# Kernel tuning notes

Hardware: AMD Instinct MI355X
Metric: run time of the kernel (lower is better)

Reference implementation:

```python
import jax, jax.numpy as jnp
import numpy as np

N_NODES = 20000
N_EDGES = 100000
MUL = 128          # channels per irrep
R = 8              # radial (edge scalar) features
H = 64             # radial MLP hidden width
SILU_NORM = 1.6790390826      # e3nn normalize2mom constant for SiLU
INV_SQRT3 = 1.0 / np.sqrt(3.0)   # wigner-3j values for l<=1 paths
PW_0E = np.sqrt(0.5)   # e3nn path weight: out dim 1, fan-in 2 paths
PW_1O = np.sqrt(1.5)   # e3nn path weight: out dim 3, fan-in 2 paths


def setup_inputs() -> dict:
    key = jax.random.key(0)
    ks = jax.random.split(key, 12)
    return dict(
        node_feats=jax.random.normal(ks[0], (N_NODES, 4 * MUL), jnp.float32),
        edge_attrs=jax.random.normal(ks[1], (N_EDGES, 4), jnp.float32),   # SH: 1x0e+1x1o
        edge_feats=jax.random.normal(ks[2], (N_EDGES, R), jnp.float32),
        edge_index=jax.random.randint(ks[3], (2, N_EDGES), 0, N_NODES),
        W_up_s=jax.random.normal(ks[4], (MUL, MUL), jnp.float32),
        W_up_v=jax.random.normal(ks[5], (MUL, MUL), jnp.float32),
        mlp_w0=jax.random.normal(ks[6], (R, H), jnp.float32),
        mlp_w1=jax.random.normal(ks[7], (H, H), jnp.float32),
        mlp_w2=jax.random.normal(ks[8], (H, H), jnp.float32),
        mlp_w3=jax.random.normal(ks[9], (H, 4 * MUL), jnp.float32),
        W_out_s=jax.random.normal(ks[10], (2 * MUL, MUL), jnp.float32),
        W_out_v=jax.random.normal(ks[11], (2 * MUL, MUL), jnp.float32),
    )


def reference(node_feats, edge_attrs, edge_feats, edge_index,
              W_up_s, W_up_v, mlp_w0, mlp_w1, mlp_w2, mlp_w3,
              W_out_s, W_out_v):
    sender = edge_index[0]
    # split node feats into irrep blocks: 128x0e then 128x1o (channel-major [u, m])
    s = node_feats[:, :MUL]                       # [N, 128]
    v = node_feats[:, MUL:].reshape(-1, MUL, 3)   # [N, 128, 3]
    # linear_up: per-irrep e3nn Linear, fan_in-normalized
    s = (s @ W_up_s) / np.sqrt(MUL)
    v = jnp.einsum('nui,uw->nwi', v, W_up_v) / np.sqrt(MUL)
    # radial MLP -> per-edge tensor-product weights (e3nn FullyConnectedNet)
    act = lambda x: jax.nn.silu(x) * SILU_NORM
    h = act(edge_feats @ (mlp_w0 / np.sqrt(R)))
    h = act(h @ (mlp_w1 / np.sqrt(H)))
    h = act(h @ (mlp_w2 / np.sqrt(H)))
    tpw = h @ (mlp_w3 / np.sqrt(H))               # [E, 4*128]
    w00, w01, w10, w11 = jnp.split(tpw, 4, axis=1)  # instruction order of weight_numel
    # gather sender node features per edge
    ss = s[sender]                                # [E, 128]
    vs = v[sender]                                # [E, 128, 3]
    sh0 = edge_attrs[:, :1]                       # [E, 1]  scalar SH
    sh1 = edge_attrs[:, 1:]                       # [E, 3]  l=1 SH
    # uvu CG tensor product paths (l<=1 wigner-3j)
    a0 = PW_0E * w00 * ss * sh0                                   # 0e x 0e -> 0e
    a1 = (PW_1O * INV_SQRT3) * (w01 * ss)[:, :, None] * sh1[:, None, :]   # 0e x 1o -> 1o
    b1 = (PW_1O * INV_SQRT3) * (w10 * sh0)[:, :, None] * vs              # 1o x 0e -> 1o
    b0 = (PW_0E * INV_SQRT3) * w11 * jnp.einsum('eui,ei->eu', vs, sh1)   # 1o x 1o -> 0e
    # irreps_mid sorted+simplified: 256x0e + 256x1o
    mid_s = jnp.concatenate([a0, b0], axis=1)     # [E, 256]
    mid_v = jnp.concatenate([a1, b1], axis=1)     # [E, 256, 3]
    # final per-irrep linear to target 128x0e + 128x1o
    out_s = (mid_s @ W_out_s) / np.sqrt(2 * MUL)
    out_v = jnp.einsum('eui,uw->ewi', mid_v, W_out_v) / np.sqrt(2 * MUL)
    return jnp.concatenate([out_s, out_v.reshape(out_v.shape[0], 3 * MUL)], axis=1)
```

## Files before the change

kernel.cpp:

```cpp
#include <hip/hip_runtime.h>
#include <stdint.h>

#define N_NODES 20000
#define N_EDGES 100000

typedef __bf16 bf16;
typedef bf16  bf16x8 __attribute__((ext_vector_type(8)));
typedef float f32x4  __attribute__((ext_vector_type(4)));

__device__ __forceinline__ f32x4 mfma16(bf16x8 a, bf16x8 b, f32x4 c) {
  return __builtin_amdgcn_mfma_f32_16x16x32_bf16(a, b, c, 0, 0, 0);
}

__device__ __forceinline__ float silu_(float y) {
  return y / (1.0f + __expf(-y));
}

#define OFF_W0T   0u
#define OFF_W1T   4096u
#define OFF_W2T   12288u
#define OFF_W3T   20480u
#define OFF_WOS   86016u
#define OFF_WOV   151552u
#define OFF_WST   217088u
#define OFF_WVT   249856u
#define OFF_SUP   282624u
#define OFF_VUP   5402624u

__global__ __launch_bounds__(256) void k0_prep(
    const float* __restrict__ wus, const float* __restrict__ wuv,
    const float* __restrict__ w0,  const float* __restrict__ w1,
    const float* __restrict__ w2,  const float* __restrict__ w3,
    const float* __restrict__ wos_g, const float* __restrict__ wov_g,
    char* __restrict__ ws) {
  const int idx = blockIdx.x * 256 + threadIdx.x;
  bf16* W0T = (bf16*)(ws + OFF_W0T);
  bf16* W1T = (bf16*)(ws + OFF_W1T);
  bf16* W2T = (bf16*)(ws + OFF_W2T);
  bf16* W3T = (bf16*)(ws + OFF_W3T);
  bf16* WOS = (bf16*)(ws + OFF_WOS);
  bf16* WOV = (bf16*)(ws + OFF_WOV);
  bf16* WST = (bf16*)(ws + OFF_WST);
  bf16* WVT = (bf16*)(ws + OFF_WVT);

  const float cS   = 0.08838834764831845f;
  const float c0   = 0.35355339059327373f;
  const float c12  = 1.6790390826f / 8.0f;
  const float cosA = 0.04419417382415922f;
  const float cosB = 0.025515518153991442f;
  const float cov  = 0.04419417382415922f;

  if (idx < 16384) {
    int w = idx >> 7, u = idx & 127;
    WST[idx] = (bf16)(wus[u * 128 + w] * cS);
    WVT[idx] = (bf16)(wuv[u * 128 + w] * cS);
  }
  if (idx < 2048) {
    int h = idx >> 5, r = idx & 31;
    W0T[idx] = (bf16)((r < 8) ? w0[r * 64 + h] * c0 : 0.0f);
  }
  if (idx < 4096) {
    int h = idx >> 6, k = idx & 63;
    W1T[idx] = (bf16)(w1[k * 64 + h] * c12);
    W2T[idx] = (bf16)(w2[k * 64 + h] * c12);
  }
  {
    int j = idx >> 6, k = idx & 63;
    W3T[idx] = (bf16)(w3[k * 512 + j] * c12);
    int w = idx >> 8, u = idx & 255;
    WOS[idx] = (bf16)(wos_g[u * 128 + w] * ((u < 128) ? cosA : cosB));
    WOV[idx] = (bf16)(wov_g[u * 128 + w] * cov);
  }
}

__global__ __launch_bounds__(256, 4) void k1_nodeup(const float* __restrict__ nf,
                                                    char* __restrict__ ws) {
  __shared__ __align__(16) bf16 tiles[4][32 * 136];
  const int n0 = blockIdx.x * 32;
  const int t = threadIdx.x;

  #pragma unroll
  for (int p = 0; p < 16; p++) {
    int idx = p * 256 + t;
    int r = idx >> 7, c4 = idx & 127;
    const float4 f = *(const float4*)&nf[(size_t)(n0 + r) * 512 + c4 * 4];
    float vals[4] = {f.x, f.y, f.z, f.w};
    #pragma unroll
    for (int e2 = 0; e2 < 4; e2++) {
      int g = c4 * 4 + e2;
      if (g < 128) {
        tiles[0][r * 136 + g] = (bf16)vals[e2];
      } else {
        int gg = g - 128;
        int u = gg / 3, i = gg - 3 * u;
        tiles[1 + i][r * 136 + u] = (bf16)vals[e2];
      }
    }
  }
  __syncthreads();

  const int wv = t >> 6, lane = t & 63;
  const int m = lane & 15, q = lane >> 4;
  const bf16* BT = (const bf16*)(ws + ((wv == 0) ? OFF_WST : OFF_WVT));
  const bf16* At = tiles[wv];

  const f32x4 z = {0.f, 0.f, 0.f, 0.f};
  f32x4 acc[2][8] = {{z, z, z, z, z, z, z, z}, {z, z, z, z, z, z, z, z}};
  #pragma unroll
  for (int kk = 0; kk < 128; kk += 32) {
    bf16x8 af0 = *(const bf16x8*)&At[m * 136 + kk + q * 8];
    bf16x8 af1 = *(const bf16x8*)&At[(16 + m) * 136 + kk + q * 8];
    #pragma unroll
    for (int nt = 0; nt < 8; nt++) {
      bf16x8 bfr = *(const bf16x8*)&BT[(nt * 16 + m) * 128 + kk + q * 8];
      acc[0][nt] = mfma16(af0, bfr, acc[0][nt]);
      acc[1][nt] = mfma16(af1, bfr, acc[1][nt]);
    }
  }

  bf16* sup = (bf16*)(ws + OFF_SUP);
  bf16* vup = (bf16*)(ws + OFF_VUP);
  #pragma unroll
  for (int rt = 0; rt < 2; rt++) {
    #pragma unroll
    for (int nt = 0; nt < 8; nt++) {
      int col = nt * 16 + m;
      #pragma unroll
      for (int r = 0; r < 4; r++) {
        int node = n0 + rt * 16 + q * 4 + r;
        if (wv == 0) sup[node * 128 + col] = (bf16)acc[rt][nt][r];
        else         vup[node * 384 + (wv - 1) * 128 + col] = (bf16)acc[rt][nt][r];
      }
    }
  }
}

#define L_TPW   0
#define L_H0    0
#define L_H1    4608
#define L_SUP   16896
#define L_VUP   25088
#define L_TOT   49664
#define TPW_LD  264

#define GLOAD_LDS16(gsrc, ldst) __builtin_amdgcn_global_load_lds( \
    (const __attribute__((address_space(1))) void*)(gsrc),        \
    (__attribute__((address_space(3))) void*)(ldst), 16, 0, 0)

__device__ __forceinline__ bf16x8 ldsw8(const bf16* row, int elem, int sw) {
  int c = elem >> 3;
  int cs = (c & ~7) | ((c ^ sw) & 7);
  return *(const bf16x8*)&row[cs * 8];
}

__device__ __forceinline__ bf16x8 build_frag(
    int wv, int ii, int kc, int off ,
    const bf16* tpr, const bf16* supR, const bf16* vupR, int sw,
    float4 at, float s1i) {
  bf16x8 af;
  if (kc < 2) {
    const int K = kc * 64 + off;
    bf16x8 sv = ldsw8(supR, K, sw);
    if (wv == 0) {
      bf16x8 tv = *(const bf16x8*)&tpr[K];
      #pragma unroll
      for (int j = 0; j < 8; j++)
        af[j] = (bf16)((float)tv[j] * (float)sv[j] * at.x);
    } else {
      bf16x8 tv = *(const bf16x8*)&tpr[128 + K];
      #pragma unroll
      for (int j = 0; j < 8; j++)
        af[j] = (bf16)((float)tv[j] * (float)sv[j] * s1i);
    }
  } else {
    const int Kl = (kc - 2) * 64 + off;
    if (wv == 0) {
      bf16x8 tv = *(const bf16x8*)&tpr[128 + Kl];
      bf16x8 vx = ldsw8(vupR, Kl, sw);
      bf16x8 vy = ldsw8(vupR, 128 + Kl, sw);
      bf16x8 vz = ldsw8(vupR, 256 + Kl, sw);
      #pragma unroll
      for (int j = 0; j < 8; j++) {
        float dv = (float)vx[j] * at.y + (float)vy[j] * at.z + (float)vz[j] * at.w;
        af[j] = (bf16)((float)tv[j] * dv);
      }
    } else {
      bf16x8 tv = *(const bf16x8*)&tpr[Kl];
      bf16x8 vv = ldsw8(vupR, ii * 128 + Kl, sw);
      #pragma unroll
      for (int j = 0; j < 8; j++)
        af[j] = (bf16)((float)tv[j] * at.x * (float)vv[j]);
    }
  }
  return af;
}

__global__ __launch_bounds__(256, 3) void k23_fused(
    const float* __restrict__ efeat, const float* __restrict__ attrs,
    const int* __restrict__ sender, const char* __restrict__ ws,
    float* __restrict__ out) {
  __shared__ __align__(16) char smem[L_TOT];
  bf16* tpwH = (bf16*)(smem + L_TPW);
  bf16* h0   = (bf16*)(smem + L_H0);
  bf16* h1   = (bf16*)(smem + L_H1);
  bf16* supL = (bf16*)(smem + L_SUP);
  bf16* vupL = (bf16*)(smem + L_VUP);

  const int e0 = blockIdx.x * 32;
  const int t = threadIdx.x;
  const int wv = t >> 6, lane = t & 63;
  const int m = lane & 15, q = lane >> 4;
  const f32x4 z = {0.f, 0.f, 0.f, 0.f};

  {
    #pragma unroll
    for (int jj = 0; jj < 2; jj++) {
      int j = wv * 2 + jj;
      int f = j * 64 + lane;
      int e = f >> 4, c = f & 15;
      int se = sender[e0 + e];
      int cs = c ^ (e & 7);
      GLOAD_LDS16(ws + OFF_SUP + (size_t)se * 256 + cs * 16,
                  (char*)supL + j * 1024);
    }
    #pragma unroll
    for (int jj = 0; jj < 6; jj++) {
      int j = wv * 6 + jj;
      int f = j * 64 + lane;
      int e = f / 48, c = f - e * 48;
      int se = sender[e0 + e];
      int cs = (c & ~7) | ((c ^ e) & 7);
      GLOAD_LDS16(ws + OFF_VUP + (size_t)se * 768 + cs * 16,
                  (char*)vupL + j * 1024);
    }
  }

  const bf16* W0T = (const bf16*)(ws + OFF_W0T);
  const bf16* W1T = (const bf16*)(ws + OFF_W1T);
  const bf16* W2T = (const bf16*)(ws + OFF_W2T);
  const bf16* W3T = (const bf16*)(ws + OFF_W3T);

  const int rt = wv & 1, nh = wv >> 1;

  {
    bf16x8 af;
    #pragma unroll
    for (int j = 0; j < 8; j++) af[j] = (bf16)0.0f;
    if (q == 0) {
      const float4* ef4 = (const float4*)efeat;
      float4 u0 = ef4[(size_t)(e0 + rt * 16 + m) * 2 + 0];
      float4 u1 = ef4[(size_t)(e0 + rt * 16 + m) * 2 + 1];
      af[0] = (bf16)u0.x; af[1] = (bf16)u0.y; af[2] = (bf16)u0.z; af[3] = (bf16)u0.w;
      af[4] = (bf16)u1.x; af[5] = (bf16)u1.y; af[6] = (bf16)u1.z; af[7] = (bf16)u1.w;
    }
    f32x4 acc[2] = {z, z};
    #pragma unroll
    for (int ntl = 0; ntl < 2; ntl++) {
      bf16x8 bfr = *(const bf16x8*)&W0T[((nh * 2 + ntl) * 16 + m) * 32 + q * 8];
      acc[ntl] = mfma16(af, bfr, acc[ntl]);
    }
    #pragma unroll
    for (int ntl = 0; ntl < 2; ntl++)
      #pragma unroll
      for (int r = 0; r < 4; r++)
        h0[(rt * 16 + q * 4 + r) * 72 + (nh * 2 + ntl) * 16 + m] = (bf16)silu_(acc[ntl][r]);
  }
  __syncthreads();

  {
    f32x4 acc[2] = {z, z};
    #pragma unroll
    for (int kk = 0; kk < 64; kk += 32) {
      bf16x8 af = *(const bf16x8*)&h0[(rt * 16 + m) * 72 + kk + q * 8];
      #pragma unroll
      for (int ntl = 0; ntl < 2; ntl++) {
        bf16x8 bfr = *(const bf16x8*)&W1T[((nh * 2 + ntl) * 16 + m) * 64 + kk + q * 8];
        acc[ntl] = mfma16(af, bfr, acc[ntl]);
      }
    }
    #pragma unroll
    for (int ntl = 0; ntl < 2; ntl++)
      #pragma unroll
      for (int r = 0; r < 4; r++)
        h1[(rt * 16 + q * 4 + r) * 72 + (nh * 2 + ntl) * 16 + m] = (bf16)silu_(acc[ntl][r]);
  }
  __syncthreads();

  {
    f32x4 acc[2] = {z, z};
    #pragma unroll
    for (int kk = 0; kk < 64; kk += 32) {
      bf16x8 af = *(const bf16x8*)&h1[(rt * 16 + m) * 72 + kk + q * 8];
      #pragma unroll
      for (int ntl = 0; ntl < 2; ntl++) {
        bf16x8 bfr = *(const bf16x8*)&W2T[((nh * 2 + ntl) * 16 + m) * 64 + kk + q * 8];
        acc[ntl] = mfma16(af, bfr, acc[ntl]);
      }
    }
    __syncthreads();
    #pragma unroll
    for (int ntl = 0; ntl < 2; ntl++)
      #pragma unroll
      for (int r = 0; r < 4; r++)
        h0[(rt * 16 + q * 4 + r) * 72 + (nh * 2 + ntl) * 16 + m] = (bf16)silu_(acc[ntl][r]);
  }
  __syncthreads();

  bf16x8 hf0 = *(const bf16x8*)&h0[(rt * 16 + m) * 72 + 0  + q * 8];
  bf16x8 hf1 = *(const bf16x8*)&h0[(rt * 16 + m) * 72 + 32 + q * 8];
  __syncthreads();

  const int eA = m, eB = 16 + m;
  const int sw = m & 7;
  const float4* at4 = (const float4*)attrs;
  const float4 atA = at4[e0 + eA];
  const float4 atB = at4[e0 + eB];
  const int ii = wv - 1;
  const float s1A = (ii == 0) ? atA.y : ((ii == 1) ? atA.z : atA.w);
  const float s1B = (ii == 0) ? atB.y : ((ii == 1) ? atB.z : atB.w);
  const bf16* tprA = tpwH + eA * TPW_LD;
  const bf16* tprB = tpwH + eB * TPW_LD;
  const bf16* supA = supL + eA * 128;
  const bf16* supB = supL + eB * 128;
  const bf16* vupA = vupL + eA * 384;
  const bf16* vupB = vupL + eB * 384;
  const bf16* WB = (const bf16*)(ws + ((wv == 0) ? OFF_WOS : OFF_WOV));

  f32x4 acc0[8] = {z, z, z, z, z, z, z, z};
  f32x4 acc1[8] = {z, z, z, z, z, z, z, z};

  #pragma unroll
  for (int half = 0; half < 2; half++) {
    if (half) __syncthreads();

    {
      #pragma unroll 2
      for (int i = 0; i < 8; i++) {
        int ntg = (wv >> 1) * 8 + i;
        f32x4 acc = z;
        const bf16* wb = &W3T[(size_t)((half * 16 + ntg) * 16 + m) * 64 + q * 8];
        bf16x8 b0 = *(const bf16x8*)&wb[0];
        bf16x8 b1 = *(const bf16x8*)&wb[32];
        acc = mfma16(hf0, b0, acc);
        acc = mfma16(hf1, b1, acc);
        #pragma unroll
        for (int r = 0; r < 4; r++)
          tpwH[(rt * 16 + q * 4 + r) * TPW_LD + ntg * 16 + m] = (bf16)acc[r];
      }
    }
    __syncthreads();

    #pragma unroll
    for (int kci = 0; kci < 2; kci++) {
      const int kc = half * 2 + kci;
      const int kb = kc * 64;
      #pragma unroll
      for (int kk = 0; kk < 64; kk += 32) {
        bf16x8 af0 = build_frag(wv, ii, kc, kk + q * 8, tprA, supA, vupA, sw, atA, s1A);
        bf16x8 af1 = build_frag(wv, ii, kc, kk + q * 8, tprB, supB, vupB, sw, atB, s1B);
        #pragma unroll
        for (int nt = 0; nt < 8; nt++) {
          bf16x8 bfr = *(const bf16x8*)&WB[(nt * 16 + m) * 256 + kb + kk + q * 8];
          acc0[nt] = mfma16(af0, bfr, acc0[nt]);
          acc1[nt] = mfma16(af1, bfr, acc1[nt]);
        }
      }
    }
  }

  #pragma unroll
  for (int b = 0; b < 2; b++) {
    const f32x4* accp = b ? acc1 : acc0;
    int rb = wv * 32 + b * 16 + q * 4;
    #pragma unroll
    for (int nt = 0; nt < 8; nt++) {
      int col = nt * 16 + m;
      #pragma unroll
      for (int r = 0; r < 4; r++) {
        int row = rb + r;
        float v = accp[nt][r];
        if (wv == 0) {
          out[(size_t)(e0 + row) * 512 + col] = v;
        } else {
          int i2 = (row - 32) >> 5, eL2 = (row - 32) & 31;
          out[(size_t)(e0 + eL2) * 512 + 128 + 3 * col + i2] = v;
        }
      }
    }
  }
}

extern "C" void kernel_launch(void* const* d_in, const int* in_sizes, int n_in,
                              void* d_out, int out_size, void* d_ws, size_t ws_size,
                              hipStream_t stream) {
  const float* node_feats = (const float*)d_in[0];
  const float* edge_attrs = (const float*)d_in[1];
  const float* edge_feats = (const float*)d_in[2];
  const int*   edge_index = (const int*)d_in[3];
  const float* W_up_s = (const float*)d_in[4];
  const float* W_up_v = (const float*)d_in[5];
  const float* w0 = (const float*)d_in[6];
  const float* w1 = (const float*)d_in[7];
  const float* w2 = (const float*)d_in[8];
  const float* w3 = (const float*)d_in[9];
  const float* Wos = (const float*)d_in[10];
  const float* Wov = (const float*)d_in[11];
  float* out = (float*)d_out;
  char* ws = (char*)d_ws;

  k0_prep<<<dim3(128), dim3(256), 0, stream>>>(W_up_s, W_up_v, w0, w1, w2, w3,
                                               Wos, Wov, ws);
  k1_nodeup<<<dim3(625), dim3(256), 0, stream>>>(node_feats, ws);
  k23_fused<<<dim3(3125), dim3(256), 0, stream>>>(edge_feats, edge_attrs,
                                                  edge_index, ws, out);
}
```

Measured before the change: 464.5 us.

## Halve edges per block in fused edge kernel to raise occupancy

The fused radial-MLP plus tensor-product kernel now handles 16 edges per block instead of 32, doubling the grid. LDS use shrinks because the per-block buffers are smaller and the tpw buffer no longer overlaps the MLP buffers. Each wave keeps one accumulator set instead of two, and launch bounds rise to 5 blocks per SM. This trades weight-fragment reuse, since each B fragment now feeds one MFMA instead of two, for more resident waves to hide gather latency.

```diff
diff --git a/kernel.cpp b/kernel.cpp
--- a/kernel.cpp
+++ b/kernel.cpp
@@ -135,13 +135,13 @@
   }
 }
 
+#define TPW_LD  264
 #define L_TPW   0
-#define L_H0    0
-#define L_H1    4608
-#define L_SUP   16896
-#define L_VUP   25088
-#define L_TOT   49664
-#define TPW_LD  264
+#define L_H0    8448
+#define L_H1    10752
+#define L_SUP   13056
+#define L_VUP   17152
+#define L_TOT   29440
 
 #define GLOAD_LDS16(gsrc, ldst) __builtin_amdgcn_global_load_lds( \
     (const __attribute__((address_space(1))) void*)(gsrc),        \
@@ -195,7 +195,7 @@
   return af;
 }
 
-__global__ __launch_bounds__(256, 3) void k23_fused(
+__global__ __launch_bounds__(256, 5) void k23_fused(
     const float* __restrict__ efeat, const float* __restrict__ attrs,
     const int* __restrict__ sender, const char* __restrict__ ws,
     float* __restrict__ out) {
@@ -206,7 +206,7 @@
   bf16* supL = (bf16*)(smem + L_SUP);
   bf16* vupL = (bf16*)(smem + L_VUP);
 
-  const int e0 = blockIdx.x * 32;
+  const int e0 = blockIdx.x * 16;
   const int t = threadIdx.x;
   const int wv = t >> 6, lane = t & 63;
   const int m = lane & 15, q = lane >> 4;
@@ -214,24 +214,22 @@
 
   {
     #pragma unroll
-    for (int jj = 0; jj < 2; jj++) {
-      int j = wv * 2 + jj;
-      int f = j * 64 + lane;
-      int e = f >> 4, c = f & 15;
-      int se = sender[e0 + e];
-      int cs = c ^ (e & 7);
-      GLOAD_LDS16(ws + OFF_SUP + (size_t)se * 256 + cs * 16,
-                  (char*)supL + j * 1024);
-    }
-    #pragma unroll
-    for (int jj = 0; jj < 6; jj++) {
-      int j = wv * 6 + jj;
-      int f = j * 64 + lane;
-      int e = f / 48, c = f - e * 48;
-      int se = sender[e0 + e];
-      int cs = (c & ~7) | ((c ^ e) & 7);
-      GLOAD_LDS16(ws + OFF_VUP + (size_t)se * 768 + cs * 16,
-                  (char*)vupL + j * 1024);
+    for (int j = 0; j < 4; j++) {
+      if (j == 0) {
+        int f = wv * 64 + lane;
+        int e = f >> 4, c = f & 15;
+        int se = sender[e0 + e];
+        int cs = (c & ~7) | ((c ^ (e & 7)) & 7);
+        GLOAD_LDS16(ws + OFF_SUP + (size_t)se * 256 + cs * 16,
+                    (char*)supL + (size_t)(wv * 64) * 16);
+      } else {
+        int v = (j - 1) * 256 + wv * 64 + lane;
+        int e = v / 48, c = v - e * 48;
+        int se = sender[e0 + e];
+        int cs = (c & ~7) | ((c ^ (e & 7)) & 7);
+        GLOAD_LDS16(ws + OFF_VUP + (size_t)se * 768 + cs * 16,
+                    (char*)vupL + (size_t)((j - 1) * 256 + wv * 64) * 16);
+      }
     }
   }
 
@@ -240,112 +238,85 @@
   const bf16* W2T = (const bf16*)(ws + OFF_W2T);
   const bf16* W3T = (const bf16*)(ws + OFF_W3T);
 
-  const int rt = wv & 1, nh = wv >> 1;
-
   {
     bf16x8 af;
     #pragma unroll
     for (int j = 0; j < 8; j++) af[j] = (bf16)0.0f;
     if (q == 0) {
       const float4* ef4 = (const float4*)efeat;
-      float4 u0 = ef4[(size_t)(e0 + rt * 16 + m) * 2 + 0];
-      float4 u1 = ef4[(size_t)(e0 + rt * 16 + m) * 2 + 1];
+      float4 u0 = ef4[(size_t)(e0 + m) * 2 + 0];
+      float4 u1 = ef4[(size_t)(e0 + m) * 2 + 1];
       af[0] = (bf16)u0.x; af[1] = (bf16)u0.y; af[2] = (bf16)u0.z; af[3] = (bf16)u0.w;
       af[4] = (bf16)u1.x; af[5] = (bf16)u1.y; af[6] = (bf16)u1.z; af[7] = (bf16)u1.w;
     }
-    f32x4 acc[2] = {z, z};
-    #pragma unroll
-    for (int ntl = 0; ntl < 2; ntl++) {
-      bf16x8 bfr = *(const bf16x8*)&W0T[((nh * 2 + ntl) * 16 + m) * 32 + q * 8];
-      acc[ntl] = mfma16(af, bfr, acc[ntl]);
-    }
-    #pragma unroll
-    for (int ntl = 0; ntl < 2; ntl++)
-      #pragma unroll
-      for (int r = 0; r < 4; r++)
-        h0[(rt * 16 + q * 4 + r) * 72 + (nh * 2 + ntl) * 16 + m] = (bf16)silu_(acc[ntl][r]);
+    f32x4 acc = z;
+    bf16x8 bfr = *(const bf16x8*)&W0T[(wv * 16 + m) * 32 + q * 8];
+    acc = mfma16(af, bfr, acc);
+    #pragma unroll
+    for (int r = 0; r < 4; r++)
+      h0[(q * 4 + r) * 72 + wv * 16 + m] = (bf16)silu_(acc[r]);
   }
   __syncthreads();
 
   {
-    f32x4 acc[2] = {z, z};
+    f32x4 acc = z;
     #pragma unroll
     for (int kk = 0; kk < 64; kk += 32) {
-      bf16x8 af = *(const bf16x8*)&h0[(rt * 16 + m) * 72 + kk + q * 8];
-      #pragma unroll
-      for (int ntl = 0; ntl < 2; ntl++) {
-        bf16x8 bfr = *(const bf16x8*)&W1T[((nh * 2 + ntl) * 16 + m) * 64 + kk + q * 8];
-        acc[ntl] = mfma16(af, bfr, acc[ntl]);
-      }
-    }
-    #pragma unroll
-    for (int ntl = 0; ntl < 2; ntl++)
-      #pragma unroll
-      for (int r = 0; r < 4; r++)
-        h1[(rt * 16 + q * 4 + r) * 72 + (nh * 2 + ntl) * 16 + m] = (bf16)silu_(acc[ntl][r]);
+      bf16x8 af = *(const bf16x8*)&h0[m * 72 + kk + q * 8];
+      bf16x8 bfr = *(const bf16x8*)&W1T[(wv * 16 + m) * 64 + kk + q * 8];
+      acc = mfma16(af, bfr, acc);
+    }
+    #pragma unroll
+    for (int r = 0; r < 4; r++)
+      h1[(q * 4 + r) * 72 + wv * 16 + m] = (bf16)silu_(acc[r]);
   }
   __syncthreads();
 
   {
-    f32x4 acc[2] = {z, z};
+    f32x4 acc = z;
     #pragma unroll
     for (int kk = 0; kk < 64; kk += 32) {
-      bf16x8 af = *(const bf16x8*)&h1[(rt * 16 + m) * 72 + kk + q * 8];
-      #pragma unroll
-      for (int ntl = 0; ntl < 2; ntl++) {
-        bf16x8 bfr = *(const bf16x8*)&W2T[((nh * 2 + ntl) * 16 + m) * 64 + kk + q * 8];
-        acc[ntl] = mfma16(af, bfr, acc[ntl]);
-      }
-    }
-    __syncthreads();
-    #pragma unroll
-    for (int ntl = 0; ntl < 2; ntl++)
-      #pragma unroll
-      for (int r = 0; r < 4; r++)
-        h0[(rt * 16 + q * 4 + r) * 72 + (nh * 2 + ntl) * 16 + m] = (bf16)silu_(acc[ntl][r]);
+      bf16x8 af = *(const bf16x8*)&h1[m * 72 + kk + q * 8];
+      bf16x8 bfr = *(const bf16x8*)&W2T[(wv * 16 + m) * 64 + kk + q * 8];
+      acc = mfma16(af, bfr, acc);
+    }
+    #pragma unroll
+    for (int r = 0; r < 4; r++)
+      h0[(q * 4 + r) * 72 + wv * 16 + m] = (bf16)silu_(acc[r]);
   }
   __syncthreads();
 
-  bf16x8 hf0 = *(const bf16x8*)&h0[(rt * 16 + m) * 72 + 0  + q * 8];
-  bf16x8 hf1 = *(const bf16x8*)&h0[(rt * 16 + m) * 72 + 32 + q * 8];
-  __syncthreads();
-
-  const int eA = m, eB = 16 + m;
+  const int eA = m;
   const int sw = m & 7;
-  const float4* at4 = (const float4*)attrs;
-  const float4 atA = at4[e0 + eA];
-  const float4 atB = at4[e0 + eB];
+  const float4 atA = ((const float4*)attrs)[e0 + eA];
   const int ii = wv - 1;
   const float s1A = (ii == 0) ? atA.y : ((ii == 1) ? atA.z : atA.w);
-  const float s1B = (ii == 0) ? atB.y : ((ii == 1) ? atB.z : atB.w);
   const bf16* tprA = tpwH + eA * TPW_LD;
-  const bf16* tprB = tpwH + eB * TPW_LD;
   const bf16* supA = supL + eA * 128;
-  const bf16* supB = supL + eB * 128;
   const bf16* vupA = vupL + eA * 384;
-  const bf16* vupB = vupL + eB * 384;
   const bf16* WB = (const bf16*)(ws + ((wv == 0) ? OFF_WOS : OFF_WOV));
 
-  f32x4 acc0[8] = {z, z, z, z, z, z, z, z};
-  f32x4 acc1[8] = {z, z, z, z, z, z, z, z};
+  f32x4 acc[8] = {z, z, z, z, z, z, z, z};
 
   #pragma unroll
   for (int half = 0; half < 2; half++) {
     if (half) __syncthreads();
 
     {
-      #pragma unroll 2
-      for (int i = 0; i < 8; i++) {
-        int ntg = (wv >> 1) * 8 + i;
-        f32x4 acc = z;
-        const bf16* wb = &W3T[(size_t)((half * 16 + ntg) * 16 + m) * 64 + q * 8];
+      bf16x8 hf0 = *(const bf16x8*)&h0[m * 72 + 0  + q * 8];
+      bf16x8 hf1 = *(const bf16x8*)&h0[m * 72 + 32 + q * 8];
+      #pragma unroll
+      for (int i = 0; i < 4; i++) {
+        int ctl = wv * 4 + i;
+        f32x4 a3 = z;
+        const bf16* wb = &W3T[(size_t)((half * 16 + ctl) * 16 + m) * 64 + q * 8];
         bf16x8 b0 = *(const bf16x8*)&wb[0];
         bf16x8 b1 = *(const bf16x8*)&wb[32];
-        acc = mfma16(hf0, b0, acc);
-        acc = mfma16(hf1, b1, acc);
+        a3 = mfma16(hf0, b0, a3);
+        a3 = mfma16(hf1, b1, a3);
         #pragma unroll
         for (int r = 0; r < 4; r++)
-          tpwH[(rt * 16 + q * 4 + r) * TPW_LD + ntg * 16 + m] = (bf16)acc[r];
+          tpwH[(q * 4 + r) * TPW_LD + ctl * 16 + m] = (bf16)a3[r];
       }
     }
     __syncthreads();
@@ -356,35 +327,27 @@
       const int kb = kc * 64;
       #pragma unroll
       for (int kk = 0; kk < 64; kk += 32) {
-        bf16x8 af0 = build_frag(wv, ii, kc, kk + q * 8, tprA, supA, vupA, sw, atA, s1A);
-        bf16x8 af1 = build_frag(wv, ii, kc, kk + q * 8, tprB, supB, vupB, sw, atB, s1B);
+        bf16x8 af = build_frag(wv, ii, kc, kk + q * 8, tprA, supA, vupA, sw, atA, s1A);
         #pragma unroll
         for (int nt = 0; nt < 8; nt++) {
           bf16x8 bfr = *(const bf16x8*)&WB[(nt * 16 + m) * 256 + kb + kk + q * 8];
-          acc0[nt] = mfma16(af0, bfr, acc0[nt]);
-          acc1[nt] = mfma16(af1, bfr, acc1[nt]);
+          acc[nt] = mfma16(af, bfr, acc[nt]);
         }
       }
     }
   }
 
   #pragma unroll
-  for (int b = 0; b < 2; b++) {
-    const f32x4* accp = b ? acc1 : acc0;
-    int rb = wv * 32 + b * 16 + q * 4;
-    #pragma unroll
-    for (int nt = 0; nt < 8; nt++) {
-      int col = nt * 16 + m;
-      #pragma unroll
-      for (int r = 0; r < 4; r++) {
-        int row = rb + r;
-        float v = accp[nt][r];
-        if (wv == 0) {
-          out[(size_t)(e0 + row) * 512 + col] = v;
-        } else {
-          int i2 = (row - 32) >> 5, eL2 = (row - 32) & 31;
-          out[(size_t)(e0 + eL2) * 512 + 128 + 3 * col + i2] = v;
-        }
+  for (int nt = 0; nt < 8; nt++) {
+    int col = nt * 16 + m;
+    #pragma unroll
+    for (int r = 0; r < 4; r++) {
+      int edge = q * 4 + r;
+      float v = acc[nt][r];
+      if (wv == 0) {
+        out[(size_t)(e0 + edge) * 512 + col] = v;
+      } else {
+        out[(size_t)(e0 + edge) * 512 + 128 + 3 * col + (wv - 1)] = v;
       }
     }
   }
@@ -411,6 +374,6 @@
   k0_prep<<<dim3(128), dim3(256), 0, stream>>>(W_up_s, W_up_v, w0, w1, w2, w3,
                                                Wos, Wov, ws);
   k1_nodeup<<<dim3(625), dim3(256), 0, stream>>>(node_feats, ws);
-  k23_fused<<<dim3(3125), dim3(256), 0, stream>>>(edge_feats, edge_attrs,
+  k23_fused<<<dim3(6250), dim3(256), 0, stream>>>(edge_feats, edge_attrs,
                                                   edge_index, ws, out);
 }
```

After: 512.1 us. +10.2%, slower.

## Split fused edge kernel into MLP/tensor-product and output-GEMM kernels via workspace

Applied to the files above, without the earlier changes.

Splits the fused per-edge kernel into two. The first runs the radial MLP and tensor product and writes bf16 mid features (1024 values per edge) to a workspace buffer. The second loads those rows with global_load_lds and performs the output linear as a GEMM of 64 rows by 256 K, with one grid column per output irrep component. The aim is to simplify the fragment-building inner loop and raise MFMA utilization, at the cost of roughly 200MB of extra global write plus read traffic. Edges are processed in chunks sized to fit the available workspace.

```diff
diff --git a/kernel.cpp b/kernel.cpp
--- a/kernel.cpp
+++ b/kernel.cpp
@@ -26,6 +26,7 @@
 #define OFF_WVT   249856u
 #define OFF_SUP   282624u
 #define OFF_VUP   5402624u
+#define OFF_MID   20762624u
 
 __global__ __launch_bounds__(256) void k0_prep(
     const float* __restrict__ wus, const float* __restrict__ wuv,
@@ -135,106 +136,21 @@
   }
 }
 
-#define L_TPW   0
-#define L_H0    0
-#define L_H1    4608
-#define L_SUP   16896
-#define L_VUP   25088
-#define L_TOT   49664
-#define TPW_LD  264
-
-#define GLOAD_LDS16(gsrc, ldst) __builtin_amdgcn_global_load_lds( \
-    (const __attribute__((address_space(1))) void*)(gsrc),        \
-    (__attribute__((address_space(3))) void*)(ldst), 16, 0, 0)
-
-__device__ __forceinline__ bf16x8 ldsw8(const bf16* row, int elem, int sw) {
-  int c = elem >> 3;
-  int cs = (c & ~7) | ((c ^ sw) & 7);
-  return *(const bf16x8*)&row[cs * 8];
-}
-
-__device__ __forceinline__ bf16x8 build_frag(
-    int wv, int ii, int kc, int off ,
-    const bf16* tpr, const bf16* supR, const bf16* vupR, int sw,
-    float4 at, float s1i) {
-  bf16x8 af;
-  if (kc < 2) {
-    const int K = kc * 64 + off;
-    bf16x8 sv = ldsw8(supR, K, sw);
-    if (wv == 0) {
-      bf16x8 tv = *(const bf16x8*)&tpr[K];
-      #pragma unroll
-      for (int j = 0; j < 8; j++)
-        af[j] = (bf16)((float)tv[j] * (float)sv[j] * at.x);
-    } else {
-      bf16x8 tv = *(const bf16x8*)&tpr[128 + K];
-      #pragma unroll
-      for (int j = 0; j < 8; j++)
-        af[j] = (bf16)((float)tv[j] * (float)sv[j] * s1i);
-    }
-  } else {
-    const int Kl = (kc - 2) * 64 + off;
-    if (wv == 0) {
-      bf16x8 tv = *(const bf16x8*)&tpr[128 + Kl];
-      bf16x8 vx = ldsw8(vupR, Kl, sw);
-      bf16x8 vy = ldsw8(vupR, 128 + Kl, sw);
-      bf16x8 vz = ldsw8(vupR, 256 + Kl, sw);
-      #pragma unroll
-      for (int j = 0; j < 8; j++) {
-        float dv = (float)vx[j] * at.y + (float)vy[j] * at.z + (float)vz[j] * at.w;
-        af[j] = (bf16)((float)tv[j] * dv);
-      }
-    } else {
-      bf16x8 tv = *(const bf16x8*)&tpr[Kl];
-      bf16x8 vv = ldsw8(vupR, ii * 128 + Kl, sw);
-      #pragma unroll
-      for (int j = 0; j < 8; j++)
-        af[j] = (bf16)((float)tv[j] * at.x * (float)vv[j]);
-    }
-  }
-  return af;
-}
-
-__global__ __launch_bounds__(256, 3) void k23_fused(
+#define TPW_LD 520
+__global__ __launch_bounds__(256, 3) void k23a_mlp_tp(
     const float* __restrict__ efeat, const float* __restrict__ attrs,
-    const int* __restrict__ sender, const char* __restrict__ ws,
-    float* __restrict__ out) {
-  __shared__ __align__(16) char smem[L_TOT];
-  bf16* tpwH = (bf16*)(smem + L_TPW);
-  bf16* h0   = (bf16*)(smem + L_H0);
-  bf16* h1   = (bf16*)(smem + L_H1);
-  bf16* supL = (bf16*)(smem + L_SUP);
-  bf16* vupL = (bf16*)(smem + L_VUP);
-
-  const int e0 = blockIdx.x * 32;
+    const int* __restrict__ sender, char* __restrict__ ws, int ebase) {
+  __shared__ __align__(16) bf16 tpw[32 * TPW_LD];
+  __shared__ __align__(16) bf16 h0[32 * 72];
+  __shared__ __align__(16) bf16 h1[32 * 72];
+
+  const int e0l = blockIdx.x * 32;
+  const int e0g = ebase + e0l;
   const int t = threadIdx.x;
   const int wv = t >> 6, lane = t & 63;
   const int m = lane & 15, q = lane >> 4;
   const f32x4 z = {0.f, 0.f, 0.f, 0.f};
 
-  {
-    #pragma unroll
-    for (int jj = 0; jj < 2; jj++) {
-      int j = wv * 2 + jj;
-      int f = j * 64 + lane;
-      int e = f >> 4, c = f & 15;
-      int se = sender[e0 + e];
-      int cs = c ^ (e & 7);
-      GLOAD_LDS16(ws + OFF_SUP + (size_t)se * 256 + cs * 16,
-                  (char*)supL + j * 1024);
-    }
-    #pragma unroll
-    for (int jj = 0; jj < 6; jj++) {
-      int j = wv * 6 + jj;
-      int f = j * 64 + lane;
-      int e = f / 48, c = f - e * 48;
-      int se = sender[e0 + e];
-      int cs = (c & ~7) | ((c ^ e) & 7);
-      GLOAD_LDS16(ws + OFF_VUP + (size_t)se * 768 + cs * 16,
-                  (char*)vupL + j * 1024);
-    }
-  }
-
   const bf16* W0T = (const bf16*)(ws + OFF_W0T);
   const bf16* W1T = (const bf16*)(ws + OFF_W1T);
   const bf16* W2T = (const bf16*)(ws + OFF_W2T);
@@ -248,8 +164,8 @@
     for (int j = 0; j < 8; j++) af[j] = (bf16)0.0f;
     if (q == 0) {
       const float4* ef4 = (const float4*)efeat;
-      float4 u0 = ef4[(size_t)(e0 + rt * 16 + m) * 2 + 0];
-      float4 u1 = ef4[(size_t)(e0 + rt * 16 + m) * 2 + 1];
+      float4 u0 = ef4[(size_t)(e0g + rt * 16 + m) * 2 + 0];
+      float4 u1 = ef4[(size_t)(e0g + rt * 16 + m) * 2 + 1];
       af[0] = (bf16)u0.x; af[1] = (bf16)u0.y; af[2] = (bf16)u0.z; af[3] = (bf16)u0.w;
       af[4] = (bf16)u1.x; af[5] = (bf16)u1.y; af[6] = (bf16)u1.z; af[7] = (bf16)u1.w;
     }
@@ -306,85 +222,129 @@
   }
   __syncthreads();
 
-  bf16x8 hf0 = *(const bf16x8*)&h0[(rt * 16 + m) * 72 + 0  + q * 8];
-  bf16x8 hf1 = *(const bf16x8*)&h0[(rt * 16 + m) * 72 + 32 + q * 8];
-  __syncthreads();
-
-  const int eA = m, eB = 16 + m;
-  const int sw = m & 7;
-  const float4* at4 = (const float4*)attrs;
-  const float4 atA = at4[e0 + eA];
-  const float4 atB = at4[e0 + eB];
-  const int ii = wv - 1;
-  const float s1A = (ii == 0) ? atA.y : ((ii == 1) ? atA.z : atA.w);
-  const float s1B = (ii == 0) ? atB.y : ((ii == 1) ? atB.z : atB.w);
-  const bf16* tprA = tpwH + eA * TPW_LD;
-  const bf16* tprB = tpwH + eB * TPW_LD;
-  const bf16* supA = supL + eA * 128;
-  const bf16* supB = supL + eB * 128;
-  const bf16* vupA = vupL + eA * 384;
-  const bf16* vupB = vupL + eB * 384;
-  const bf16* WB = (const bf16*)(ws + ((wv == 0) ? OFF_WOS : OFF_WOV));
-
-  f32x4 acc0[8] = {z, z, z, z, z, z, z, z};
-  f32x4 acc1[8] = {z, z, z, z, z, z, z, z};
-
-  #pragma unroll
-  for (int half = 0; half < 2; half++) {
-    if (half) __syncthreads();
-
-    {
-      #pragma unroll 2
-      for (int i = 0; i < 8; i++) {
-        int ntg = (wv >> 1) * 8 + i;
-        f32x4 acc = z;
-        const bf16* wb = &W3T[(size_t)((half * 16 + ntg) * 16 + m) * 64 + q * 8];
-        bf16x8 b0 = *(const bf16x8*)&wb[0];
-        bf16x8 b1 = *(const bf16x8*)&wb[32];
-        acc = mfma16(hf0, b0, acc);
-        acc = mfma16(hf1, b1, acc);
-        #pragma unroll
-        for (int r = 0; r < 4; r++)
-          tpwH[(rt * 16 + q * 4 + r) * TPW_LD + ntg * 16 + m] = (bf16)acc[r];
-      }
-    }
-    __syncthreads();
-
-    #pragma unroll
-    for (int kci = 0; kci < 2; kci++) {
-      const int kc = half * 2 + kci;
-      const int kb = kc * 64;
-      #pragma unroll
-      for (int kk = 0; kk < 64; kk += 32) {
-        bf16x8 af0 = build_frag(wv, ii, kc, kk + q * 8, tprA, supA, vupA, sw, atA, s1A);
-        bf16x8 af1 = build_frag(wv, ii, kc, kk + q * 8, tprB, supB, vupB, sw, atB, s1B);
-        #pragma unroll
-        for (int nt = 0; nt < 8; nt++) {
-          bf16x8 bfr = *(const bf16x8*)&WB[(nt * 16 + m) * 256 + kb + kk + q * 8];
-          acc0[nt] = mfma16(af0, bfr, acc0[nt]);
-          acc1[nt] = mfma16(af1, bfr, acc1[nt]);
-        }
-      }
-    }
-  }
-
-  #pragma unroll
-  for (int b = 0; b < 2; b++) {
-    const f32x4* accp = b ? acc1 : acc0;
-    int rb = wv * 32 + b * 16 + q * 4;
+  {
+    bf16x8 hf0 = *(const bf16x8*)&h0[(rt * 16 + m) * 72 + 0  + q * 8];
+    bf16x8 hf1 = *(const bf16x8*)&h0[(rt * 16 + m) * 72 + 32 + q * 8];
+    #pragma unroll 4
+    for (int i = 0; i < 16; i++) {
+      int ntg = nh * 16 + i;
+      f32x4 a3 = z;
+      const bf16* wb = &W3T[(size_t)(ntg * 16 + m) * 64 + q * 8];
+      bf16x8 b0 = *(const bf16x8*)&wb[0];
+      bf16x8 b1 = *(const bf16x8*)&wb[32];
+      a3 = mfma16(hf0, b0, a3);
+      a3 = mfma16(hf1, b1, a3);
+      #pragma unroll
+      for (int r = 0; r < 4; r++)
+        tpw[(rt * 16 + q * 4 + r) * TPW_LD + ntg * 16 + m] = (bf16)a3[r];
+    }
+  }
+  __syncthreads();
+
+  const int e  = t >> 3;
+  const int uc = t & 7;
+  const int se = sender[e0g + e];
+  const float4 at = ((const float4*)attrs)[e0g + e];
+  const bf16* tpr  = tpw + e * TPW_LD;
+  const bf16* supR = (const bf16*)(ws + OFF_SUP) + (size_t)se * 128;
+  const bf16* vupR = (const bf16*)(ws + OFF_VUP) + (size_t)se * 384;
+  bf16* midp = (bf16*)(ws + OFF_MID) + (size_t)(e0l + e) * 1024;
+
+  #pragma unroll
+  for (int c = 0; c < 2; c++) {
+    const int u0 = uc * 16 + c * 8;
+    bf16x8 w00 = *(const bf16x8*)&tpr[u0];
+    bf16x8 w01 = *(const bf16x8*)&tpr[128 + u0];
+    bf16x8 w10 = *(const bf16x8*)&tpr[256 + u0];
+    bf16x8 w11 = *(const bf16x8*)&tpr[384 + u0];
+    bf16x8 sv = *(const bf16x8*)&supR[u0];
+    bf16x8 vx = *(const bf16x8*)&vupR[u0];
+    bf16x8 vy = *(const bf16x8*)&vupR[128 + u0];
+    bf16x8 vz = *(const bf16x8*)&vupR[256 + u0];
+    bf16x8 osa, osb, ova0, ovb0, ova1, ovb1, ova2, ovb2;
+    #pragma unroll
+    for (int j = 0; j < 8; j++) {
+      float fw00 = (float)w00[j], fw01 = (float)w01[j];
+      float fw10 = (float)w10[j], fw11 = (float)w11[j];
+      float fsv = (float)sv[j];
+      float fvx = (float)vx[j], fvy = (float)vy[j], fvz = (float)vz[j];
+      osa[j]  = (bf16)(fw00 * fsv * at.x);
+      osb[j]  = (bf16)(fw11 * (fvx * at.y + fvy * at.z + fvz * at.w));
+      ova0[j] = (bf16)(fw01 * fsv * at.y);
+      ova1[j] = (bf16)(fw01 * fsv * at.z);
+      ova2[j] = (bf16)(fw01 * fsv * at.w);
+      ovb0[j] = (bf16)(fw10 * at.x * fvx);
+      ovb1[j] = (bf16)(fw10 * at.x * fvy);
+      ovb2[j] = (bf16)(fw10 * at.x * fvz);
+    }
+    *(bf16x8*)&midp[u0]             = osa;
+    *(bf16x8*)&midp[128 + u0]       = osb;
+    *(bf16x8*)&midp[256 + u0]       = ova0;
+    *(bf16x8*)&midp[256 + 128 + u0] = ovb0;
+    *(bf16x8*)&midp[512 + u0]       = ova1;
+    *(bf16x8*)&midp[512 + 128 + u0] = ovb1;
+    *(bf16x8*)&midp[768 + u0]       = ova2;
+    *(bf16x8*)&midp[768 + 128 + u0] = ovb2;
+  }
+}
+
+#define GLOAD_LDS16(gsrc, ldst) __builtin_amdgcn_global_load_lds( \
+    (const __attribute__((address_space(1))) void*)(gsrc),        \
+    (__attribute__((address_space(3))) void*)(ldst), 16, 0, 0)
+
+__global__ __launch_bounds__(256, 3) void k23b_out(
+    const char* __restrict__ ws, float* __restrict__ out,
+    int ebase, int ecount) {
+  __shared__ __align__(16) bf16 Als[64 * 256];
+  const int st = blockIdx.y;
+  const int r0 = blockIdx.x * 64;
+  const int t = threadIdx.x;
+  const int wv = t >> 6, lane = t & 63;
+  const int m = lane & 15, q = lane >> 4;
+  const f32x4 z = {0.f, 0.f, 0.f, 0.f};
+
+  const char* mid = ws + OFF_MID;
+
+  #pragma unroll
+  for (int j = 0; j < 8; j++) {
+    int g = (j * 4 + wv) * 64 + lane;
+    int r = g >> 5, c5 = g & 31;
+    int er = r0 + r; if (er >= ecount) er = ecount - 1;
+    int cs = (c5 & ~7) | ((c5 ^ (r & 7)) & 7);
+    GLOAD_LDS16(mid + (size_t)er * 2048 + (size_t)st * 512 + cs * 16,
+                (char*)Als + (size_t)((j * 4 + wv) * 64) * 16);
+  }
+  __syncthreads();
+
+  const bf16* WB = (const bf16*)(ws + ((st == 0) ? OFF_WOS : OFF_WOV));
+  const int R = wv * 16 + m;
+  const int rsw = R & 7;
+
+  f32x4 acc[8] = {z, z, z, z, z, z, z, z};
+  #pragma unroll
+  for (int kk8 = 0; kk8 < 8; kk8++) {
+    const int kk = kk8 * 32;
+    const int cl = kk8 * 4 + q;
+    const int cp = (cl & ~7) | ((cl ^ rsw) & 7);
+    bf16x8 af = *(const bf16x8*)&Als[R * 256 + cp * 8];
     #pragma unroll
     for (int nt = 0; nt < 8; nt++) {
-      int col = nt * 16 + m;
-      #pragma unroll
-      for (int r = 0; r < 4; r++) {
-        int row = rb + r;
-        float v = accp[nt][r];
-        if (wv == 0) {
-          out[(size_t)(e0 + row) * 512 + col] = v;
-        } else {
-          int i2 = (row - 32) >> 5, eL2 = (row - 32) & 31;
-          out[(size_t)(e0 + eL2) * 512 + 128 + 3 * col + i2] = v;
-        }
+      bf16x8 bfr = *(const bf16x8*)&WB[(size_t)(nt * 16 + m) * 256 + kk + q * 8];
+      acc[nt] = mfma16(af, bfr, acc[nt]);
+    }
+  }
+
+  #pragma unroll
+  for (int nt = 0; nt < 8; nt++) {
+    int col = nt * 16 + m;
+    #pragma unroll
+    for (int r = 0; r < 4; r++) {
+      int le = r0 + wv * 16 + q * 4 + r;
+      if (le < ecount) {
+        float v = acc[nt][r];
+        size_t row = (size_t)(ebase + le) * 512;
+        if (st == 0) out[row + col] = v;
+        else         out[row + 128 + 3 * col + (st - 1)] = v;
       }
     }
   }
@@ -411,6 +371,16 @@
   k0_prep<<<dim3(128), dim3(256), 0, stream>>>(W_up_s, W_up_v, w0, w1, w2, w3,
                                                Wos, Wov, ws);
   k1_nodeup<<<dim3(625), dim3(256), 0, stream>>>(node_feats, ws);
-  k23_fused<<<dim3(3125), dim3(256), 0, stream>>>(edge_feats, edge_attrs,
-                                                  edge_index, ws, out);
-}
+
+  long cap = (ws_size > (size_t)OFF_MID) ? (long)(ws_size - OFF_MID) : 0;
+  long epc = (cap / 2048) & ~31L;
+  if (epc > N_EDGES) epc = N_EDGES;
+  if (epc < 32) epc = 32;
+  for (long eb = 0; eb < N_EDGES; eb += epc) {
+    long ec = N_EDGES - eb; if (ec > epc) ec = epc;
+    k23a_mlp_tp<<<dim3((unsigned)(ec / 32)), dim3(256), 0, stream>>>(
+        edge_feats, edge_attrs, edge_index, ws, (int)eb);
+    k23b_out<<<dim3((unsigned)((ec + 63) / 64), 4), dim3(256), 0, stream>>>(
+        ws, out, (int)eb, (int)ec);
+  }
+}
```

After: 647.0 us. 1.39x slower.
